# Kernel optimization log

Hardware: AMD Instinct MI355X
Metric: run time of the kernel (lower is better)

Reference implementation:

```python
import jax, jax.numpy as jnp
import numpy as np

THETA = 10000.0
D_K = 128
B, S = 16, 8192


def setup_inputs() -> dict:
    key = jax.random.key(0)
    k1, k2 = jax.random.split(key)
    x = jax.random.normal(k1, (B, S, D_K), dtype=jnp.float32)
    # Original module ignores token_positions, but it is a required forward arg.
    token_positions = jnp.sort(jax.random.randint(k2, (B, S), 0, S), axis=-1).astype(jnp.int32)
    return {"x": x, "token_positions": token_positions}


def reference(x, token_positions):
    # Faithful to the source: rotation[j] is indexed by the SEQUENCE index j,
    # token_positions is ignored. Block-diagonal 2x2 rotation on consecutive
    # pairs (x[2k], x[2k+1]) with angle = pos / theta**(2k/d), applied as R @ x.
    seq = x.shape[1]
    d = x.shape[-1]
    half = d // 2
    pos = jnp.arange(seq, dtype=x.dtype)                      # [S]
    inv_freq = THETA ** (-(2.0 * jnp.arange(half, dtype=x.dtype)) / d)  # [half]
    ang = pos[:, None] * inv_freq                             # [S, half]
    cos = jnp.cos(ang)                                        # [S, half]
    sin = jnp.sin(ang)
    xe = x[..., 0::2]                                         # [B, S, half]
    xo = x[..., 1::2]
    oe = xe * cos - xo * sin
    oo = xe * sin + xo * cos
    # re-interleave pairs back to [B, S, D]
    return jnp.stack([oe, oo], axis=-1).reshape(x.shape)
```

## Files before the change

kernel.cpp:

```cpp
#include <hip/hip_runtime.h>
#include <math.h>


constexpr int B_DIM = 16;
constexpr int S_DIM = 8192;
constexpr int D_DIM = 128;

#define LOG2_THETA_OVER_HALFD 0.20762050593046014f

__global__ __launch_bounds__(256) void rope_kernel(const float4* __restrict__ x,
                                                   float4* __restrict__ out) {
    const int g = blockIdx.x * blockDim.x + threadIdx.x;
    const int j = g & 31;
    const int row = g >> 5;
    const int s = row & (S_DIM - 1);

    const float4 v = x[g];

    const float fi0 = (float)(2 * j);
    const float fi1 = fi0 + 1.0f;
    const float inv0 = exp2f(-fi0 * LOG2_THETA_OVER_HALFD);
    const float inv1 = exp2f(-fi1 * LOG2_THETA_OVER_HALFD);

    const float fs = (float)s;
    float s0, c0, s1, c1;
    __sincosf(fs * inv0, &s0, &c0);
    __sincosf(fs * inv1, &s1, &c1);

    float4 o;
    o.x = v.x * c0 - v.y * s0;
    o.y = v.x * s0 + v.y * c0;
    o.z = v.z * c1 - v.w * s1;
    o.w = v.z * s1 + v.w * c1;
    out[g] = o;
}

extern "C" void kernel_launch(void* const* d_in, const int* in_sizes, int n_in,
                              void* d_out, int out_size, void* d_ws, size_t ws_size,
                              hipStream_t stream) {
    const float4* x = (const float4*)d_in[0];
    float4* out = (float4*)d_out;
    const int total_f4 = B_DIM * S_DIM * (D_DIM / 4);
    const int block = 256;
    const int grid = total_f4 / block;
    rope_kernel<<<grid, block, 0, stream>>>(x, out);
}
```

Measured before the change: 110.3 us.

## Process four batch-strided vectors per thread reusing sincos, with nontemporal memory ops

Each thread now loads four float4 vectors spaced a quarter of the tensor apart (same sequence position and pair index), computes the rotation sin/cos once and applies it to all four. Loads and stores use nontemporal builtins, and the second inverse frequency is derived by multiplying by a constant instead of a second exp2f. This cuts transcendental work per element and increases outstanding memory requests per thread, at the cost of a grid four times smaller.

Result: slower. 119.6 us (+8.4%).

```diff
diff --git a/kernel.cpp b/kernel.cpp
--- a/kernel.cpp
+++ b/kernel.cpp
@@ -5,43 +5,54 @@
 constexpr int B_DIM = 16;
 constexpr int S_DIM = 8192;
 constexpr int D_DIM = 128;
+constexpr int TOTAL_F4 = B_DIM * S_DIM * (D_DIM / 4);
+constexpr int QUARTER  = TOTAL_F4 / 4;
 
-#define LOG2_THETA_OVER_HALFD 0.20762050593046014f
+#define L2T_OVER_HALFD 0.20762050593046014f
+#define KSTEP          0.8659643233600653f
 
-__global__ __launch_bounds__(256) void rope_kernel(const float4* __restrict__ x,
-                                                   float4* __restrict__ out) {
-    const int g = blockIdx.x * blockDim.x + threadIdx.x;
-    const int j = g & 31;
-    const int row = g >> 5;
-    const int s = row & (S_DIM - 1);
+typedef float vf4 __attribute__((ext_vector_type(4)));
 
-    const float4 v = x[g];
+__device__ __forceinline__ vf4 rope4(vf4 v, float s0, float c0, float s1, float c1) {
+    vf4 o;
+    o.x = v.x * c0 - v.y * s0;
+    o.y = v.x * s0 + v.y * c0;
+    o.z = v.z * c1 - v.w * s1;
+    o.w = v.z * s1 + v.w * c1;
+    return o;
+}
 
-    const float fi0 = (float)(2 * j);
-    const float fi1 = fi0 + 1.0f;
-    const float inv0 = exp2f(-fi0 * LOG2_THETA_OVER_HALFD);
-    const float inv1 = exp2f(-fi1 * LOG2_THETA_OVER_HALFD);
+__global__ __launch_bounds__(256) void rope_kernel(const vf4* __restrict__ x,
+                                                   vf4* __restrict__ out) {
+    const int t = blockIdx.x * blockDim.x + threadIdx.x;
 
+    const vf4 v0 = __builtin_nontemporal_load(&x[t]);
+    const vf4 v1 = __builtin_nontemporal_load(&x[t + QUARTER]);
+    const vf4 v2 = __builtin_nontemporal_load(&x[t + 2 * QUARTER]);
+    const vf4 v3 = __builtin_nontemporal_load(&x[t + 3 * QUARTER]);
+
+    const int j = t & 31;
+    const int s = (t >> 5) & (S_DIM - 1);
+
+    const float inv0 = exp2f(-(float)(2 * j) * L2T_OVER_HALFD);
+    const float inv1 = inv0 * KSTEP;
     const float fs = (float)s;
     float s0, c0, s1, c1;
     __sincosf(fs * inv0, &s0, &c0);
     __sincosf(fs * inv1, &s1, &c1);
 
-    float4 o;
-    o.x = v.x * c0 - v.y * s0;
-    o.y = v.x * s0 + v.y * c0;
-    o.z = v.z * c1 - v.w * s1;
-    o.w = v.z * s1 + v.w * c1;
-    out[g] = o;
+    __builtin_nontemporal_store(rope4(v0, s0, c0, s1, c1), &out[t]);
+    __builtin_nontemporal_store(rope4(v1, s0, c0, s1, c1), &out[t + QUARTER]);
+    __builtin_nontemporal_store(rope4(v2, s0, c0, s1, c1), &out[t + 2 * QUARTER]);
+    __builtin_nontemporal_store(rope4(v3, s0, c0, s1, c1), &out[t + 3 * QUARTER]);
 }
 
 extern "C" void kernel_launch(void* const* d_in, const int* in_sizes, int n_in,
                               void* d_out, int out_size, void* d_ws, size_t ws_size,
                               hipStream_t stream) {
-    const float4* x = (const float4*)d_in[0];
-    float4* out = (float4*)d_out;
-    const int total_f4 = B_DIM * S_DIM * (D_DIM / 4);
+    const vf4* x = (const vf4*)d_in[0];
+    vf4* out = (vf4*)d_out;
     const int block = 256;
-    const int grid = total_f4 / block;
+    const int grid = QUARTER / block;
     rope_kernel<<<grid, block, 0, stream>>>(x, out);
 }
```
